# Kernel tuning notes

Measured on AMD Instinct MI355X. Metric: run time of the kernel, lower is better.

## Reference

```python
import jax, jax.numpy as jnp
import numpy as np

B = 8192
IN = 1024
H = 1024


def setup_inputs() -> dict:
    key = jax.random.key(0)
    ks = jax.random.split(key, 12)
    def xavier(k, shape):
        fan_in, fan_out = shape[1], shape[0]
        std = (2.0 / (fan_in + fan_out)) ** 0.5
        return jax.random.normal(k, shape, dtype=jnp.float32) * std
    return {
        "x": jax.random.normal(ks[0], (B, IN), dtype=jnp.float32),
        "hprev": jax.random.normal(ks[1], (B, H), dtype=jnp.float32),
        "c": jax.random.normal(ks[2], (B, 2 * H), dtype=jnp.float32),
        "Wh": xavier(ks[3], (H, IN)),
        "Wz": xavier(ks[4], (H, IN)),
        "Wr": xavier(ks[5], (H, IN)),
        "Uh": xavier(ks[6], (H, H)),
        "Uz": xavier(ks[7], (H, H)),
        "Ur": xavier(ks[8], (H, H)),
        "Ch": xavier(ks[9], (H, 2 * H)),
        "Cz": xavier(ks[10], (H, 2 * H)),
        "Cr": xavier(ks[11], (H, 2 * H)),
        "bh": jnp.zeros((H,), dtype=jnp.float32),
        "bz": jnp.zeros((H,), dtype=jnp.float32),
        "br": jnp.zeros((H,), dtype=jnp.float32),
    }


def reference(x, hprev, c, Wh, Wz, Wr, Uh, Uz, Ur, Ch, Cz, Cr, bh, bz, br):
    # batch_mul(W, v) == v @ W.T for batched vectors
    r = jax.nn.sigmoid(x @ Wr.T + hprev @ Ur.T + c @ Cr.T + br)
    z = jax.nn.sigmoid(x @ Wz.T + hprev @ Uz.T + c @ Cz.T + bz)
    h_prop = jnp.tanh(x @ Wh.T + (r * hprev) @ Uh.T + c @ Ch.T + bh)
    return z * h_prop + (1.0 - z) * hprev
```

## Files before the change

kernel.cpp:

```cpp
#include <hip/hip_runtime.h>
#include <hip/hip_bf16.h>

typedef __attribute__((ext_vector_type(8))) short bf16x8;
typedef __attribute__((ext_vector_type(8))) unsigned short u16x8;
typedef __attribute__((ext_vector_type(4))) float f32x4;

#define BK 64
#define BM 128
#define BN 128

__device__ __forceinline__ unsigned short f2b(float f) {
    union { float f; unsigned int u; } x; x.f = f;
    unsigned int r = x.u + 0x7fffu + ((x.u >> 16) & 1u);
    return (unsigned short)(r >> 16);
}
__device__ __forceinline__ float b2f(unsigned short b) {
    union { unsigned int u; float f; } x; x.u = ((unsigned int)b) << 16;
    return x.f;
}
__device__ __forceinline__ float sigmoidf_(float v) {
    return 1.0f / (1.0f + __expf(-v));
}
__device__ __forceinline__ float tanhf_(float v) {
    return 1.0f - 2.0f / (__expf(2.0f * v) + 1.0f);
}

__device__ __forceinline__ void gll16(const void* g, void* l) {
    __builtin_amdgcn_global_load_lds(
        (const __attribute__((address_space(1))) void*)g,
        (__attribute__((address_space(3))) void*)l,
        16, 0, 0);
}

#define FENCE() asm volatile("" ::: "memory")
#define BARRIER() do { FENCE(); __builtin_amdgcn_s_barrier(); FENCE(); } while (0)

__global__ __launch_bounds__(512, 2) void gemm1(
    const unsigned short* __restrict__ Xall,
    const unsigned short* __restrict__ Wcat,
    const float* __restrict__ hprev,
    const float* __restrict__ br, const float* __restrict__ bz,
    unsigned short* __restrict__ rh,
    unsigned short* __restrict__ zs,
    unsigned short* __restrict__ shp0,
    unsigned short* __restrict__ shp1)
{
    __shared__ __attribute__((aligned(16))) unsigned short As[2 * 256 * BK];
    __shared__ __attribute__((aligned(16))) unsigned short Bs[2 * 256 * BK];

    const int f = blockIdx.x;
    int bm, bn, tstart, nkt, rfrom, slice = 0;
    if (f < 256) {
        bm = f >> 3; bn = f & 7;
        tstart = 0; nkt = 64; rfrom = 1 << 30;
    } else {
        const int u = f - 256;
        const int x = u & 7;
        bm = u >> 3; bn = 8 + (x >> 1); slice = x & 1;
        tstart = slice * 24; nkt = 24; rfrom = 16;
    }
    const int m0 = bm * 256;
    const int n0 = bn * 256;

    const int st  = threadIdx.x;
    const int sr  = st >> 3;
    const int scb = st & 7;
    const int ssw = (scb ^ (sr & 7)) * 8;
    const unsigned short* gA = Xall + (size_t)(m0 + sr) * 4096 + ssw;
    const unsigned short* gB = Wcat + (size_t)(n0 + sr) * 4096 + ssw;
    const int lt = sr * BK + scb * 8;

    auto k0f = [&](int tt) -> int {
        const int kp = tstart + tt;
        return kp * 64 + (kp >= rfrom ? 1024 : 0);
    };
    auto stageA = [&](int buf, int half, int k0) {
        const unsigned short* g = gA + (size_t)half * 128 * 4096 + k0;
        unsigned short* l = As + buf * (256 * BK) + half * 128 * BK + lt;
        gll16(g, l);
        gll16(g + (size_t)64 * 4096, l + 64 * BK);
    };
    auto stageB = [&](int buf, int half, int k0) {
        const unsigned short* g = gB + (size_t)half * 128 * 4096 + k0;
        unsigned short* l = Bs + buf * (256 * BK) + half * 128 * BK + lt;
        gll16(g, l);
        gll16(g + (size_t)64 * 4096, l + 64 * BK);
    };

    {
        const int k0 = k0f(0);
        stageA(0, 0, k0); stageA(0, 1, k0);
        stageB(0, 0, k0); stageB(0, 1, k0);
        const int k1 = k0f(1);
        stageB(1, 0, k1); stageB(1, 1, k1);
        stageA(1, 0, k1);
        asm volatile("s_waitcnt vmcnt(6)" ::: "memory");
        BARRIER();
    }

    const int lane = st & 63;
    const int w = st >> 6;
    const int wm = w >> 2, wn = w & 3;
    const int l15 = lane & 15, lhi = lane >> 4, lx = lane & 7;
    const int raBase = (wm * 128 + l15) * BK;
    const int rbBase = (wn * 64 + l15) * BK;
    const int off0 = (lhi ^ lx) * 8;
    const int off1 = ((4 + lhi) ^ lx) * 8;

    f32x4 acc[8][4] = {};
    bf16x8 a[4][2], b[4][2];

    for (int t = 0; t < nkt; ++t) {
        const unsigned short* Ab = As + (t & 1) * (256 * BK);
        const unsigned short* Bb = Bs + (t & 1) * (256 * BK);

        #pragma unroll
        for (int m = 0; m < 4; ++m) {
            a[m][0] = *(const bf16x8*)(Ab + raBase + m * 16 * BK + off0);
            a[m][1] = *(const bf16x8*)(Ab + raBase + m * 16 * BK + off1);
        }
        #pragma unroll
        for (int n = 0; n < 4; ++n) {
            b[n][0] = *(const bf16x8*)(Bb + rbBase + n * 16 * BK + off0);
            b[n][1] = *(const bf16x8*)(Bb + rbBase + n * 16 * BK + off1);
        }
        if (t + 1 < nkt) stageA((t + 1) & 1, 1, k0f(t + 1));
        BARRIER();
        asm volatile("s_waitcnt lgkmcnt(0)" ::: "memory");
        __builtin_amdgcn_sched_barrier(0);
        __builtin_amdgcn_s_setprio(1);
        #pragma unroll
        for (int m = 0; m < 4; ++m)
            #pragma unroll
            for (int n = 0; n < 2; ++n) {
                acc[m][n] = __builtin_amdgcn_mfma_f32_16x16x32_bf16(a[m][0], b[n][0], acc[m][n], 0, 0, 0);
                acc[m][n] = __builtin_amdgcn_mfma_f32_16x16x32_bf16(a[m][1], b[n][1], acc[m][n], 0, 0, 0);
            }
        __builtin_amdgcn_s_setprio(0);
        BARRIER();

        if (t + 2 < nkt) stageB(t & 1, 0, k0f(t + 2));
        BARRIER();
        __builtin_amdgcn_s_setprio(1);
        #pragma unroll
        for (int m = 0; m < 4; ++m)
            #pragma unroll
            for (int n = 2; n < 4; ++n) {
                acc[m][n] = __builtin_amdgcn_mfma_f32_16x16x32_bf16(a[m][0], b[n][0], acc[m][n], 0, 0, 0);
                acc[m][n] = __builtin_amdgcn_mfma_f32_16x16x32_bf16(a[m][1], b[n][1], acc[m][n], 0, 0, 0);
            }
        __builtin_amdgcn_s_setprio(0);
        BARRIER();

        #pragma unroll
        for (int m = 0; m < 4; ++m) {
            a[m][0] = *(const bf16x8*)(Ab + raBase + (64 + m * 16) * BK + off0);
            a[m][1] = *(const bf16x8*)(Ab + raBase + (64 + m * 16) * BK + off1);
        }
        if (t + 2 < nkt) stageB(t & 1, 1, k0f(t + 2));
        BARRIER();
        asm volatile("s_waitcnt lgkmcnt(0)" ::: "memory");
        __builtin_amdgcn_sched_barrier(0);
        __builtin_amdgcn_s_setprio(1);
        #pragma unroll
        for (int m = 0; m < 4; ++m)
            #pragma unroll
            for (int n = 0; n < 2; ++n) {
                acc[4 + m][n] = __builtin_amdgcn_mfma_f32_16x16x32_bf16(a[m][0], b[n][0], acc[4 + m][n], 0, 0, 0);
                acc[4 + m][n] = __builtin_amdgcn_mfma_f32_16x16x32_bf16(a[m][1], b[n][1], acc[4 + m][n], 0, 0, 0);
            }
        __builtin_amdgcn_s_setprio(0);
        BARRIER();

        if (t + 2 < nkt) stageA(t & 1, 0, k0f(t + 2));
        if (t >= nkt - 2) asm volatile("s_waitcnt vmcnt(0)" ::: "memory");
        else              asm volatile("s_waitcnt vmcnt(6)" ::: "memory");
        BARRIER();
        __builtin_amdgcn_s_setprio(1);
        #pragma unroll
        for (int m = 0; m < 4; ++m)
            #pragma unroll
            for (int n = 2; n < 4; ++n) {
                acc[4 + m][n] = __builtin_amdgcn_mfma_f32_16x16x32_bf16(a[m][0], b[n][0], acc[4 + m][n], 0, 0, 0);
                acc[4 + m][n] = __builtin_amdgcn_mfma_f32_16x16x32_bf16(a[m][1], b[n][1], acc[4 + m][n], 0, 0, 0);
            }
        __builtin_amdgcn_s_setprio(0);
        BARRIER();
    }

    const int rowb = m0 + wm * 128 + lhi * 4;
    if (f < 256) {
        const int gate = bn >> 2;
        const int colb = (n0 - gate * 1024) + wn * 64 + l15;
        if (gate == 0) {
            #pragma unroll
            for (int i = 0; i < 8; ++i)
                #pragma unroll
                for (int r = 0; r < 4; ++r) {
                    const int m = rowb + i * 16 + r;
                    #pragma unroll
                    for (int j = 0; j < 4; ++j) {
                        const int n = colb + j * 16;
                        const size_t idx = (size_t)m * 1024 + n;
                        const float rr = sigmoidf_(acc[i][j][r] + br[n]);
                        rh[idx] = f2b(rr * hprev[idx]);
                    }
                }
        } else {
            #pragma unroll
            for (int i = 0; i < 8; ++i)
                #pragma unroll
                for (int r = 0; r < 4; ++r) {
                    const int m = rowb + i * 16 + r;
                    #pragma unroll
                    for (int j = 0; j < 4; ++j) {
                        const int n = colb + j * 16;
                        const size_t idx = (size_t)m * 1024 + n;
                        zs[idx] = f2b(sigmoidf_(acc[i][j][r] + bz[n]));
                    }
                }
        }
    } else {
        unsigned short* __restrict__ dst = slice ? shp1 : shp0;
        const int colb = (n0 - 2048) + wn * 64 + l15;
        #pragma unroll
        for (int i = 0; i < 8; ++i)
            #pragma unroll
            for (int r = 0; r < 4; ++r) {
                const int m = rowb + i * 16 + r;
                #pragma unroll
                for (int j = 0; j < 4; ++j) {
                    const int n = colb + j * 16;
                    dst[(size_t)m * 1024 + n] = f2b(acc[i][j][r]);
                }
            }
    }
}

__device__ __forceinline__ void mma_core(
    const unsigned short* __restrict__ A, int lda,
    const unsigned short* __restrict__ B, int ldb,
    int m0, int n0, int nk, int remap_from, int remap_add,
    unsigned short* As, unsigned short* Bs, f32x4 acc[4][4])
{
    const int t = threadIdx.x;
    const int lane = t & 63;
    const int wm = (t >> 7) & 1;
    const int wn = (t >> 6) & 1;
    const int srow = t >> 3;
    const int ldsCol = (t & 7) * 8;
    const int swc = (((t & 7) ^ ((t >> 3) & 7))) * 8;

    for (int kt = 0; kt < nk; ++kt) {
        int k0 = kt * BK + (kt >= remap_from ? remap_add : 0);
        __syncthreads();
        #pragma unroll
        for (int j = 0; j < 4; ++j) {
            int row = j * 32 + srow;
            gll16(A + (size_t)(m0 + row) * lda + k0 + swc, As + row * BK + ldsCol);
            gll16(B + (size_t)(n0 + row) * ldb + k0 + swc, Bs + row * BK + ldsCol);
        }
        __syncthreads();
        #pragma unroll
        for (int kk = 0; kk < 2; ++kk) {
            bf16x8 af[4], bfr[4];
            const int off = (((kk * 4 + (lane >> 4)) ^ (lane & 7))) * 8;
            const int ra = (wm * 64 + (lane & 15)) * BK + off;
            const int rb = (wn * 64 + (lane & 15)) * BK + off;
            #pragma unroll
            for (int i = 0; i < 4; ++i)
                af[i] = *(const bf16x8*)(As + ra + i * 16 * BK);
            #pragma unroll
            for (int j = 0; j < 4; ++j)
                bfr[j] = *(const bf16x8*)(Bs + rb + j * 16 * BK);
            #pragma unroll
            for (int i = 0; i < 4; ++i)
                #pragma unroll
                for (int j = 0; j < 4; ++j)
                    acc[i][j] = __builtin_amdgcn_mfma_f32_16x16x32_bf16(
                        af[i], bfr[j], acc[i][j], 0, 0, 0);
        }
    }
}

__global__ __launch_bounds__(256, 4) void gemm2(
    const unsigned short* __restrict__ rh,
    const unsigned short* __restrict__ Uhb,
    const unsigned short* __restrict__ shp0,
    const unsigned short* __restrict__ shp1,
    const float* __restrict__ bh,
    const unsigned short* __restrict__ zs,
    const float* __restrict__ hprev,
    float* __restrict__ out)
{
    __shared__ __attribute__((aligned(16))) unsigned short As[BM * BK];
    __shared__ __attribute__((aligned(16))) unsigned short Bs[BN * BK];
    f32x4 acc[4][4] = {};

    const int flat = blockIdx.y * gridDim.x + blockIdx.x;
    const int xcd = flat & 7;
    const int p = flat >> 3;
    const int bm = xcd * 8 + (p & 7);
    const int bn = p >> 3;
    const int m0 = bm * BM, n0 = bn * BN;

    mma_core(rh, 1024, Uhb, 1024, m0, n0, 16, 1 << 30, 0, As, Bs, acc);

    const int lane = threadIdx.x & 63;
    const int wm = (threadIdx.x >> 7) & 1, wn = (threadIdx.x >> 6) & 1;
    const int rowb = m0 + wm * 64 + (lane >> 4) * 4;
    const int colb = n0 + wn * 64 + (lane & 15);

    #pragma unroll
    for (int i = 0; i < 4; ++i)
        #pragma unroll
        for (int r = 0; r < 4; ++r) {
            int m = rowb + i * 16 + r;
            #pragma unroll
            for (int j = 0; j < 4; ++j) {
                int n = colb + j * 16;
                size_t idx = (size_t)m * 1024 + n;
                float val = acc[i][j][r] + b2f(shp0[idx]) + b2f(shp1[idx]) + bh[n];
                float hp = tanhf_(val);
                float zv = b2f(zs[idx]);
                out[idx] = zv * hp + (1.0f - zv) * hprev[idx];
            }
        }
}

struct CastJobs {
    const float* src[12];
    unsigned short* dst[12];
    int start[13];
    int cs3[12];
    int stride[12];
};

__global__ __launch_bounds__(256) void cast_all(CastJobs jb, int total) {
    for (int i = blockIdx.x * blockDim.x + threadIdx.x; i < total;
         i += gridDim.x * blockDim.x) {
        int j = 0;
        #pragma unroll
        for (int k = 1; k < 12; ++k) j += (i >= jb.start[k]) ? 1 : 0;
        const int li = i - jb.start[j];
        const float4* src = (const float4*)jb.src[j];
        float4 a = src[2 * li];
        float4 b = src[2 * li + 1];
        const int cs3 = jb.cs3[j];
        int row = li >> cs3;
        int col = (li & ((1 << cs3) - 1)) * 8;
        u16x8 o;
        o[0] = f2b(a.x); o[1] = f2b(a.y); o[2] = f2b(a.z); o[3] = f2b(a.w);
        o[4] = f2b(b.x); o[5] = f2b(b.y); o[6] = f2b(b.z); o[7] = f2b(b.w);
        *(u16x8*)(jb.dst[j] + (size_t)row * jb.stride[j] + col) = o;
    }
}

extern "C" void kernel_launch(void* const* d_in, const int* in_sizes, int n_in,
                              void* d_out, int out_size, void* d_ws, size_t ws_size,
                              hipStream_t stream) {
    const float* x     = (const float*)d_in[0];
    const float* hprev = (const float*)d_in[1];
    const float* c     = (const float*)d_in[2];
    const float* Wh    = (const float*)d_in[3];
    const float* Wz    = (const float*)d_in[4];
    const float* Wr    = (const float*)d_in[5];
    const float* Uh    = (const float*)d_in[6];
    const float* Uz    = (const float*)d_in[7];
    const float* Ur    = (const float*)d_in[8];
    const float* Ch    = (const float*)d_in[9];
    const float* Cz    = (const float*)d_in[10];
    const float* Cr    = (const float*)d_in[11];
    const float* bh    = (const float*)d_in[12];
    const float* bz    = (const float*)d_in[13];
    const float* br    = (const float*)d_in[14];

    char* ws = (char*)d_ws;
    unsigned short* Xall = (unsigned short*)ws; ws += (size_t)8192 * 4096 * 2;
    unsigned short* Wcat = (unsigned short*)ws; ws += (size_t)3072 * 4096 * 2;
    unsigned short* Uhb  = (unsigned short*)ws; ws += (size_t)1024 * 1024 * 2;
    unsigned short* rhb  = (unsigned short*)ws; ws += (size_t)8192 * 1024 * 2;
    unsigned short* shp  = (unsigned short*)ws; ws += (size_t)8192 * 1024 * 2;
    unsigned short* zsb  = (unsigned short*)ws; ws += (size_t)8192 * 1024 * 2;
    unsigned short* shpB = (unsigned short*)ws; ws += (size_t)8192 * 1024 * 2;

    CastJobs jb;
    int acc = 0;
    auto setjob = [&](int j, const float* s, unsigned short* dbase, int col0,
                      int rows, int cols, int stride) {
        jb.src[j] = s; jb.dst[j] = dbase + col0;
        jb.start[j] = acc;
        acc += rows * cols / 8;
        jb.cs3[j] = (cols == 2048) ? 8 : 7;
        jb.stride[j] = stride;
    };
    setjob(0, x,     Xall, 0,    8192, 1024, 4096);
    setjob(1, hprev, Xall, 1024, 8192, 1024, 4096);
    setjob(2, c,     Xall, 2048, 8192, 2048, 4096);
    setjob(3, Wr, Wcat, 0,    1024, 1024, 4096);
    setjob(4, Ur, Wcat, 1024, 1024, 1024, 4096);
    setjob(5, Cr, Wcat, 2048, 1024, 2048, 4096);
    setjob(6, Wz, Wcat + 1024 * 4096, 0,    1024, 1024, 4096);
    setjob(7, Uz, Wcat + 1024 * 4096, 1024, 1024, 1024, 4096);
    setjob(8, Cz, Wcat + 1024 * 4096, 2048, 1024, 2048, 4096);
    setjob(9,  Wh, Wcat + 2048 * 4096, 0,    1024, 1024, 4096);
    setjob(10, Ch, Wcat + 2048 * 4096, 2048, 1024, 2048, 4096);
    setjob(11, Uh, Uhb, 0, 1024, 1024, 1024);
    jb.start[12] = acc;

    hipLaunchKernelGGL(cast_all, dim3(2048), dim3(256), 0, stream, jb, acc);
    hipLaunchKernelGGL(gemm1, dim3(512), dim3(512), 0, stream,
                       Xall, Wcat, hprev, br, bz, rhb, zsb, shp, shpB);
    hipLaunchKernelGGL(gemm2, dim3(8, 64), dim3(256), 0, stream,
                       rhb, Uhb, shp, shpB, bh, zsb, hprev, (float*)d_out);
}
```

Measured before the change: 459.5 us.

## Software-pipeline LDS fragment loads across MFMA quadrants with split register sets

Restructures the main GEMM loop so LDS fragment reads for the next quadrant (B high half, A high half, and the next tile's A/B low halves) are issued before or alongside the MFMA blocks of the current quadrant. Separate aLo/aHi/bLo/bHi registers replace the single a/b buffers, and the explicit lgkmcnt waits and sched_barriers are dropped so the compiler can overlap ds_reads with MFMAs. This also adds a prologue that preloads the first fragments and handles the nkt==1 case. The cost is higher register pressure from the extra fragment buffers, which may affect occupancy under the 512x2 launch bounds.

Result: slower. 480.0 us (+4.5%).

```diff
diff --git a/kernel.cpp b/kernel.cpp
--- a/kernel.cpp
+++ b/kernel.cpp
@@ -34,6 +34,18 @@
 
 #define FENCE() asm volatile("" ::: "memory")
 #define BARRIER() do { FENCE(); __builtin_amdgcn_s_barrier(); FENCE(); } while (0)
+
+#define MMAQ(MB, NB, AF, BF)                                                     \
+    _Pragma("unroll")                                                            \
+    for (int m_ = 0; m_ < 4; ++m_) {                                             \
+        _Pragma("unroll")                                                        \
+        for (int n_ = 0; n_ < 2; ++n_) {                                         \
+            acc[(MB) + m_][(NB) + n_] = __builtin_amdgcn_mfma_f32_16x16x32_bf16( \
+                AF[m_][0], BF[n_][0], acc[(MB) + m_][(NB) + n_], 0, 0, 0);       \
+            acc[(MB) + m_][(NB) + n_] = __builtin_amdgcn_mfma_f32_16x16x32_bf16( \
+                AF[m_][1], BF[n_][1], acc[(MB) + m_][(NB) + n_], 0, 0, 0);       \
+        }                                                                        \
+    }
 
 __global__ __launch_bounds__(512, 2) void gemm1(
     const unsigned short* __restrict__ Xall,
@@ -87,17 +99,6 @@
         gll16(g + (size_t)64 * 4096, l + 64 * BK);
     };
 
-    {
-        const int k0 = k0f(0);
-        stageA(0, 0, k0); stageA(0, 1, k0);
-        stageB(0, 0, k0); stageB(0, 1, k0);
-        const int k1 = k0f(1);
-        stageB(1, 0, k1); stageB(1, 1, k1);
-        stageA(1, 0, k1);
-        asm volatile("s_waitcnt vmcnt(6)" ::: "memory");
-        BARRIER();
-    }
-
     const int lane = st & 63;
     const int w = st >> 6;
     const int wm = w >> 2, wn = w & 3;
@@ -108,67 +109,67 @@
     const int off1 = ((4 + lhi) ^ lx) * 8;
 
     f32x4 acc[8][4] = {};
-    bf16x8 a[4][2], b[4][2];
+    bf16x8 aLo[4][2], aHi[4][2], bLo[2][2], bHi[2][2];
+
+    {
+        const int k0 = k0f(0);
+        stageA(0, 0, k0); stageA(0, 1, k0);
+        stageB(0, 0, k0); stageB(0, 1, k0);
+        if (nkt > 1) {
+            const int k1 = k0f(1);
+            stageA(1, 0, k1);
+            stageB(1, 0, k1); stageB(1, 1, k1);
+            asm volatile("s_waitcnt vmcnt(6)" ::: "memory");
+        } else {
+            asm volatile("s_waitcnt vmcnt(0)" ::: "memory");
+        }
+        BARRIER();
+        #pragma unroll
+        for (int m = 0; m < 4; ++m) {
+            aLo[m][0] = *(const bf16x8*)(As + raBase + m * 16 * BK + off0);
+            aLo[m][1] = *(const bf16x8*)(As + raBase + m * 16 * BK + off1);
+        }
+        #pragma unroll
+        for (int n = 0; n < 2; ++n) {
+            bLo[n][0] = *(const bf16x8*)(Bs + rbBase + n * 16 * BK + off0);
+            bLo[n][1] = *(const bf16x8*)(Bs + rbBase + n * 16 * BK + off1);
+        }
+    }
 
     for (int t = 0; t < nkt; ++t) {
         const unsigned short* Ab = As + (t & 1) * (256 * BK);
         const unsigned short* Bb = Bs + (t & 1) * (256 * BK);
+        const unsigned short* An = As + ((t + 1) & 1) * (256 * BK);
+        const unsigned short* Bn = Bs + ((t + 1) & 1) * (256 * BK);
+
+        #pragma unroll
+        for (int n = 0; n < 2; ++n) {
+            bHi[n][0] = *(const bf16x8*)(Bb + rbBase + (2 + n) * 16 * BK + off0);
+            bHi[n][1] = *(const bf16x8*)(Bb + rbBase + (2 + n) * 16 * BK + off1);
+        }
+        if (t + 1 < nkt) stageA((t + 1) & 1, 1, k0f(t + 1));
+        BARRIER();
+        __builtin_amdgcn_s_setprio(1);
+        MMAQ(0, 0, aLo, bLo);
+        __builtin_amdgcn_s_setprio(0);
+        BARRIER();
 
         #pragma unroll
         for (int m = 0; m < 4; ++m) {
-            a[m][0] = *(const bf16x8*)(Ab + raBase + m * 16 * BK + off0);
-            a[m][1] = *(const bf16x8*)(Ab + raBase + m * 16 * BK + off1);
-        }
-        #pragma unroll
-        for (int n = 0; n < 4; ++n) {
-            b[n][0] = *(const bf16x8*)(Bb + rbBase + n * 16 * BK + off0);
-            b[n][1] = *(const bf16x8*)(Bb + rbBase + n * 16 * BK + off1);
-        }
-        if (t + 1 < nkt) stageA((t + 1) & 1, 1, k0f(t + 1));
-        BARRIER();
-        asm volatile("s_waitcnt lgkmcnt(0)" ::: "memory");
-        __builtin_amdgcn_sched_barrier(0);
+            aHi[m][0] = *(const bf16x8*)(Ab + raBase + (64 + m * 16) * BK + off0);
+            aHi[m][1] = *(const bf16x8*)(Ab + raBase + (64 + m * 16) * BK + off1);
+        }
+        if (t + 2 < nkt) stageB(t & 1, 0, k0f(t + 2));
+        BARRIER();
         __builtin_amdgcn_s_setprio(1);
-        #pragma unroll
-        for (int m = 0; m < 4; ++m)
-            #pragma unroll
-            for (int n = 0; n < 2; ++n) {
-                acc[m][n] = __builtin_amdgcn_mfma_f32_16x16x32_bf16(a[m][0], b[n][0], acc[m][n], 0, 0, 0);
-                acc[m][n] = __builtin_amdgcn_mfma_f32_16x16x32_bf16(a[m][1], b[n][1], acc[m][n], 0, 0, 0);
-            }
+        MMAQ(0, 2, aLo, bHi);
         __builtin_amdgcn_s_setprio(0);
         BARRIER();
 
-        if (t + 2 < nkt) stageB(t & 1, 0, k0f(t + 2));
+        if (t + 2 < nkt) stageB(t & 1, 1, k0f(t + 2));
         BARRIER();
         __builtin_amdgcn_s_setprio(1);
-        #pragma unroll
-        for (int m = 0; m < 4; ++m)
-            #pragma unroll
-            for (int n = 2; n < 4; ++n) {
-                acc[m][n] = __builtin_amdgcn_mfma_f32_16x16x32_bf16(a[m][0], b[n][0], acc[m][n], 0, 0, 0);
-                acc[m][n] = __builtin_amdgcn_mfma_f32_16x16x32_bf16(a[m][1], b[n][1], acc[m][n], 0, 0, 0);
-            }
-        __builtin_amdgcn_s_setprio(0);
-        BARRIER();
-
-        #pragma unroll
-        for (int m = 0; m < 4; ++m) {
-            a[m][0] = *(const bf16x8*)(Ab + raBase + (64 + m * 16) * BK + off0);
-            a[m][1] = *(const bf16x8*)(Ab + raBase + (64 + m * 16) * BK + off1);
-        }
-        if (t + 2 < nkt) stageB(t & 1, 1, k0f(t + 2));
-        BARRIER();
-        asm volatile("s_waitcnt lgkmcnt(0)" ::: "memory");
-        __builtin_amdgcn_sched_barrier(0);
-        __builtin_amdgcn_s_setprio(1);
-        #pragma unroll
-        for (int m = 0; m < 4; ++m)
-            #pragma unroll
-            for (int n = 0; n < 2; ++n) {
-                acc[4 + m][n] = __builtin_amdgcn_mfma_f32_16x16x32_bf16(a[m][0], b[n][0], acc[4 + m][n], 0, 0, 0);
-                acc[4 + m][n] = __builtin_amdgcn_mfma_f32_16x16x32_bf16(a[m][1], b[n][1], acc[4 + m][n], 0, 0, 0);
-            }
+        MMAQ(4, 0, aHi, bLo);
         __builtin_amdgcn_s_setprio(0);
         BARRIER();
 
@@ -176,14 +177,20 @@
         if (t >= nkt - 2) asm volatile("s_waitcnt vmcnt(0)" ::: "memory");
         else              asm volatile("s_waitcnt vmcnt(6)" ::: "memory");
         BARRIER();
+        if (t + 1 < nkt) {
+            #pragma unroll
+            for (int m = 0; m < 4; ++m) {
+                aLo[m][0] = *(const bf16x8*)(An + raBase + m * 16 * BK + off0);
+                aLo[m][1] = *(const bf16x8*)(An + raBase + m * 16 * BK + off1);
+            }
+            #pragma unroll
+            for (int n = 0; n < 2; ++n) {
+                bLo[n][0] = *(const bf16x8*)(Bn + rbBase + n * 16 * BK + off0);
+                bLo[n][1] = *(const bf16x8*)(Bn + rbBase + n * 16 * BK + off1);
+            }
+        }
         __builtin_amdgcn_s_setprio(1);
-        #pragma unroll
-        for (int m = 0; m < 4; ++m)
-            #pragma unroll
-            for (int n = 2; n < 4; ++n) {
-                acc[4 + m][n] = __builtin_amdgcn_mfma_f32_16x16x32_bf16(a[m][0], b[n][0], acc[4 + m][n], 0, 0, 0);
-                acc[4 + m][n] = __builtin_amdgcn_mfma_f32_16x16x32_bf16(a[m][1], b[n][1], acc[4 + m][n], 0, 0, 0);
-            }
+        MMAQ(4, 2, aHi, bHi);
         __builtin_amdgcn_s_setprio(0);
         BARRIER();
     }
```
